# Optimization experiments

Hardware: AMD Instinct MI355X
Metric: run time of the kernel (lower is better)

Reference implementation:

```python
import jax, jax.numpy as jnp
import numpy as np

B, T, BIN, D, S, L = 128, 512, 24, 256, 128, 2
MAX_LEN = 512.0   # config.max_length, used as attention score scale
EPS = 1e-6
P = 3.0           # GeM pooling power


def _sinusoid(t, dim, min_ts=1.0, max_ts=10000.0):
    # half sin / half cos geometric timescales (min_timescale..max_timescale)
    num = dim // 2
    inv = min_ts * jnp.exp(jnp.arange(num, dtype=jnp.float32) * (-np.log(max_ts / min_ts) / max(num - 1, 1)))
    ang = jnp.arange(t, dtype=jnp.float32)[:, None] * inv[None, :]        # [T, dim/2]
    return jnp.concatenate([jnp.sin(ang), jnp.cos(ang)], axis=-1)          # [T, dim]


def _rope(x):
    # rotate-half RoPE over last dim, positions along axis -2
    t, d = x.shape[-2], x.shape[-1]
    inv = 1.0 / (10000.0 ** (jnp.arange(0, d, 2, dtype=jnp.float32) / d))  # [d/2]
    ang = jnp.arange(t, dtype=jnp.float32)[:, None] * inv[None, :]         # [T, d/2]
    sin = jnp.concatenate([jnp.sin(ang), jnp.sin(ang)], axis=-1)
    cos = jnp.concatenate([jnp.cos(ang), jnp.cos(ang)], axis=-1)
    x1, x2 = jnp.split(x, 2, axis=-1)
    return x * cos + jnp.concatenate([-x2, x1], axis=-1) * sin


def setup_inputs() -> dict:
    key = jax.random.key(0)
    ks = jax.random.split(key, 12)
    std_in = 1.0 / np.sqrt(BIN)
    std_d = 1.0 / np.sqrt(D)
    return {
        "x": jax.random.uniform(ks[0], (B, T, BIN), dtype=jnp.float32),
        "pe_scale": jnp.ones((), jnp.float32),                                  # learnable PE scale
        "W_in": jax.random.normal(ks[1], (BIN, D), jnp.float32) * std_in,        # encoder_start
        "b_in": jnp.zeros((D,), jnp.float32),
        "norm_scale": jnp.ones((L,), jnp.float32),                               # ScaledNorm scalar per layer
        "W1": jax.random.normal(ks[2], (L, D, 2 * D + S), jnp.float32) * std_d,  # GAU in-proj
        "b1": jnp.zeros((L, 2 * D + S), jnp.float32),
        "gamma": jnp.ones((L, 2, S), jnp.float32),                               # q/k offset-scale
        "beta": jnp.zeros((L, 2, S), jnp.float32),
        "W2": jax.random.normal(ks[3], (L, D, D), jnp.float32) * std_d,          # GAU out-proj
        "b2": jnp.zeros((L, D), jnp.float32),
        "We": jax.random.normal(ks[4], (D, D), jnp.float32) * std_d,             # metric embedding
        "be": jnp.zeros((D,), jnp.float32),
    }


def reference(x, pe_scale, W_in, b_in, norm_scale, W1, b1, gamma, beta, W2, b2, We, be):
    # scaled sinusoidal positional embedding (additive)
    h = x + pe_scale * _sinusoid(x.shape[1], x.shape[2])
    # encoder start + swish
    h = jax.nn.swish(h @ W_in + b_in)                                   # [B,T,D]
    for i in range(L):  # GAU stack (attention-free gated attention units)
        shortcut = h
        hn = h * jax.lax.rsqrt(jnp.mean(h * h, axis=-1, keepdims=True) + EPS) * norm_scale[i]
        uv = jax.nn.swish(hn @ W1[i] + b1[i])                           # [B,T,2D+S]
        u, v, base = uv[..., :D], uv[..., D:2 * D], uv[..., 2 * D:]
        q = _rope(base * gamma[i, 0] + beta[i, 0])                      # [B,T,S]
        k = _rope(base * gamma[i, 1] + beta[i, 1])
        scores = jnp.einsum('bnd,bmd->bnm', q, k) / MAX_LEN             # [B,T,T]
        attn = jnp.square(jax.nn.relu(scores))                          # SqrReLU
        out = u * jnp.einsum('bnm,bme->bne', attn, v)                   # gated attention output
        h = shortcut + out @ W2[i] + b2[i]
    unpooled = h
    # generalized-mean pooling over sequence (p=3, clamp for stability)
    pooled = jnp.mean(jnp.clip(h, EPS, None) ** P, axis=1) ** (1.0 / P)  # [B,D]
    # metric embedding: linear + L2 normalize
    emb = pooled @ We + be
    emb = emb / jnp.linalg.norm(emb, axis=-1, keepdims=True)
    return emb, unpooled
```

## Files before the change

### kernel.cpp

```cpp
#include <hip/hip_runtime.h>
#include <hip/hip_bf16.h>

#define B_ 128
#define T_ 512
#define BIN_ 24
#define D_ 256
#define S_ 128
#define L_ 2
#define BT_ (B_*T_)

typedef __hip_bfloat16 bf16;
typedef __hip_bfloat162 bf162;
typedef __attribute__((ext_vector_type(8))) short bf16x8;
typedef __attribute__((ext_vector_type(4))) short s16x4;
typedef __attribute__((ext_vector_type(4))) float f32x4;

__device__ __forceinline__ float b2f(bf16 x){ return __bfloat162float(x); }
__device__ __forceinline__ bf16 f2b(float x){ return __float2bfloat16(x); }
__device__ __forceinline__ float swish(float v){
  float e = __builtin_amdgcn_exp2f(-1.442695040888963f * v);
  return v * __builtin_amdgcn_rcpf(1.f + e);
}

__global__ void tables_kernel(const float* pe_scale_ptr, float* pe_tab, float* rs, float* rc) {
  int t = blockIdx.x;
  int j = threadIdx.x;
  float ps = pe_scale_ptr[0];
  const float LOG1E4 = 9.210340371976184f;
  if (j < 64) {
    float inv = expf(-LOG1E4 * (float)j / 64.f);
    float ang = (float)t * inv;
    rs[t*64 + j] = sinf(ang);
    rc[t*64 + j] = cosf(ang);
  }
  if (j < BIN_) {
    int jj = (j < 12) ? j : (j - 12);
    float inv = expf(-LOG1E4 * (float)jj / 11.f);
    float ang = (float)t * inv;
    pe_tab[t*BIN_ + j] = ps * ((j < 12) ? sinf(ang) : cosf(ang));
  }
}

__global__ __launch_bounds__(256) void prep_kernel(const float* W1, const float* W2,
                                                   bf16* W1t, bf16* W2t) {
  int idx = blockIdx.x*256 + threadIdx.x;
  if (idx < 2*256*640) {
    int l = idx / (256*640); int rem = idx % (256*640);
    int k = rem / 640; int n = rem % 640;
    W1t[(size_t)l*640*256 + n*256 + k] = f2b(W1[idx]);
  }
  if (idx < 2*256*256) {
    int l = idx >> 16; int rem = idx & 65535;
    int k = rem >> 8; int n = rem & 255;
    W2t[(size_t)l*65536 + n*256 + k] = f2b(W2[idx]);
  }
}

__global__ __launch_bounds__(256) void init_kernel(float* rms1, float* pooled_raw) {
  int i = blockIdx.x*256 + threadIdx.x;
  if (i < BT_) rms1[i] = 0.f;
  if (i < B_*D_) pooled_raw[i] = 0.f;
}

__global__ __launch_bounds__(256) void embed_kernel(const float* x, const float* pe_tab,
                const float* W_in, const float* b_in, float* h, float* rms0, bf16* hb) {
  __shared__ float xr[8][BIN_];
  __shared__ float wsum[4][8];
  int tid = threadIdx.x;
  int row0 = blockIdx.x * 8;
  if (tid < 8*BIN_) {
    int r = tid / BIN_, k = tid % BIN_;
    int row = row0 + r;
    int t = row & (T_-1);
    xr[r][k] = x[(size_t)row*BIN_ + k] + pe_tab[t*BIN_ + k];
  }
  __syncthreads();
  int d = tid;
  float bi = b_in[d];
  float acc[8];
  #pragma unroll
  for (int r=0;r<8;r++) acc[r]=bi;
  #pragma unroll
  for (int k=0;k<BIN_;k++){
    float w = W_in[k*D_ + d];
    #pragma unroll
    for (int r=0;r<8;r++) acc[r] += xr[r][k]*w;
  }
  float sq[8];
  #pragma unroll
  for (int r=0;r<8;r++){
    float v = swish(acc[r]);
    h[(size_t)(row0+r)*D_ + d] = v;
    hb[(size_t)(row0+r)*D_ + d] = f2b(v);
    sq[r] = v*v;
  }
  #pragma unroll
  for (int off=1; off<64; off<<=1)
    #pragma unroll
    for (int r=0;r<8;r++) sq[r] += __shfl_xor(sq[r], off);
  if ((tid&63)==0)
    #pragma unroll
    for (int r=0;r<8;r++) wsum[tid>>6][r] = sq[r];
  __syncthreads();
  if (tid < 8) rms0[row0+tid] = wsum[0][tid]+wsum[1][tid]+wsum[2][tid]+wsum[3][tid];
}

__global__ __launch_bounds__(256) void gemm1_mfma(const bf16* A, const bf16* Bt,
      const float* bias, const float* rmsraw, const float* norm_scale, int l,
      bf16* u, bf16* Vtg, bf16* basebuf) {
  __shared__ bf16 As[128*72];
  __shared__ bf16 Bs[128*72];
  bf16* Ovl = As;

  int tid = threadIdx.x;
  int w = tid>>6, lane = tid&63, r = lane&15, g = lane>>4;
  int wr = w>>1, wc = w&1;
  int dd = blockIdx.x; int xcd = dd&7, slot = dd>>3;
  int panel = xcd*64 + slot/5; int bx = slot%5;
  int row0 = panel*128, col0 = bx*128;

  f32x4 acc[4][4];
  #pragma unroll
  for (int i=0;i<4;i++)
    #pragma unroll
    for (int j=0;j<4;j++) acc[i][j] = (f32x4){0.f,0.f,0.f,0.f};

  for (int k0=0; k0<D_; k0+=64) {
    #pragma unroll
    for (int i=0;i<4;i++){
      int id = i*256 + tid; int tr = id>>3, tc = id&7;
      *(bf16x8*)(As + tr*72 + tc*8) = *(const bf16x8*)(A  + (size_t)(row0+tr)*D_ + k0 + tc*8);
      *(bf16x8*)(Bs + tr*72 + tc*8) = *(const bf16x8*)(Bt + (size_t)(col0+tr)*D_ + k0 + tc*8);
    }
    __syncthreads();
    #pragma unroll
    for (int kk=0; kk<2; kk++){
      bf16x8 a[4], b[4];
      #pragma unroll
      for (int i=0;i<4;i++){
        a[i] = *(const bf16x8*)(As + (64*wr+16*i+r)*72 + kk*32 + g*8);
        b[i] = *(const bf16x8*)(Bs + (64*wc+16*i+r)*72 + kk*32 + g*8);
      }
      #pragma unroll
      for (int i=0;i<4;i++)
        #pragma unroll
        for (int j=0;j<4;j++)
          acc[i][j] = __builtin_amdgcn_mfma_f32_16x16x32_bf16(a[i], b[j], acc[i][j], 0,0,0);
    }
    __syncthreads();
  }

  float ns = norm_scale[l];
  #pragma unroll
  for (int i=0;i<4;i++){
    size_t grow0 = row0 + 64*wr + 16*i + 4*g;
    float4 rv = *(const float4*)(rmsraw + grow0);
    float sc[4];
    sc[0] = rsqrtf(rv.x*(1.f/D_) + 1e-6f) * ns;
    sc[1] = rsqrtf(rv.y*(1.f/D_) + 1e-6f) * ns;
    sc[2] = rsqrtf(rv.z*(1.f/D_) + 1e-6f) * ns;
    sc[3] = rsqrtf(rv.w*(1.f/D_) + 1e-6f) * ns;
    #pragma unroll
    for (int j=0;j<4;j++){
      int gcol = col0 + 64*wc + 16*j + r;
      float bv = bias[gcol];
      if (bx < 2) {
        #pragma unroll
        for (int reg=0; reg<4; reg++){
          float v = swish(acc[i][j][reg]*sc[reg] + bv);
          u[(grow0+reg)*D_ + gcol] = f2b(v);
        }
      } else if (bx < 4) {
        #pragma unroll
        for (int reg=0; reg<4; reg++){
          float v = swish(acc[i][j][reg]*sc[reg] + bv);
          Ovl[(64*wc+16*j+r)*136 + (64*wr+16*i+4*g+reg)] = f2b(v);
        }
      } else {
        #pragma unroll
        for (int reg=0; reg<4; reg++){
          float v = swish(acc[i][j][reg]*sc[reg] + bv);
          basebuf[(grow0+reg)*S_ + (gcol-512)] = f2b(v);
        }
      }
    }
  }

  if (bx == 2 || bx == 3) {
    __syncthreads();
    size_t bb = row0 >> 9;
    int mg = row0 & 511;
    #pragma unroll
    for (int c=0;c<8;c++){
      int chunk = c*256 + tid;
      int e = chunk >> 4, mloc = (chunk & 15)*8;
      *(bf16x8*)(Vtg + bb*131072 + (size_t)(col0-256+e)*T_ + mg + mloc) =
        *(const bf16x8*)(Ovl + e*136 + mloc);
    }
  }
}

__global__ __launch_bounds__(256) void qk_kernel(const bf16* basebuf, const float* gamma, const float* beta,
      int l, const float* rs, const float* rc, bf16* q, bf16* k) {
  int tid = threadIdx.x;
  int j = tid & 127;
  size_t row = (size_t)blockIdx.x*2 + (tid>>7);
  int t = (int)(row & (T_-1));
  int j2 = j ^ 64;
  float v0 = b2f(basebuf[row*S_ + j]);
  float v1 = b2f(basebuf[row*S_ + j2]);
  int jm = j & 63;
  float sn = rs[t*64 + jm], cs = rc[t*64 + jm];
  float sgn = (j < 64) ? -1.f : 1.f;
  const float* g  = gamma + l*2*S_;
  const float* bt = beta  + l*2*S_;
  float xq = v0*g[j]      + bt[j];
  float pq = v1*g[j2]     + bt[j2];
  q[row*S_ + j] = f2b(xq*cs + sgn*pq*sn);
  float xk = v0*g[S_+j]   + bt[S_+j];
  float pk = v1*g[S_+j2]  + bt[S_+j2];
  k[row*S_ + j] = f2b(xk*cs + sgn*pk*sn);
}

__global__ __launch_bounds__(512, 4) void attn_gemm2_fused(const bf16* q, const bf16* k,
      const bf16* Vtg, const bf16* u, const bf16* W2t, const float* bias,
      float* h, int mode, float* rms1, float* pooled_raw, float* outb, bf16* hb) {
  __shared__ char smem[77824];
  bf16* Ks = (bf16*)smem;
  bf16* Vt = (bf16*)(smem + 17408);
  bf16* Ps = (bf16*)(smem + 50176);
  bf16* Os = (bf16*)smem;
  bf16* Wt = (bf16*)(smem + 67584);

  int tid = threadIdx.x;
  int w = tid >> 6, l = tid & 63;
  int r = l & 15, g = l >> 4;
  int xcd = blockIdx.x & 7, j0 = blockIdx.x >> 3;
  int b  = xcd*16 + (j0 >> 2);
  int nt = j0 & 3;
  size_t rowbase = (size_t)b * T_;
  int n0 = nt * 128;

  bf16x8 qf[4];
  const bf16* qrow = q + (rowbase + n0 + 16*w + r) * S_ + g*8;
  #pragma unroll
  for (int kk=0; kk<4; kk++) qf[kk] = *(const bf16x8*)(qrow + kk*32);

  f32x4 oacc[16];
  #pragma unroll
  for (int i=0;i<16;i++) oacc[i] = (f32x4){0.f,0.f,0.f,0.f};

  for (int m0 = 0; m0 < T_; m0 += 64) {
    #pragma unroll
    for (int i=0;i<2;i++){
      int chunk = i*512 + tid;
      int row = chunk >> 4, c = chunk & 15;
      *(bf16x8*)(Ks + row*136 + c*8) =
        *(const bf16x8*)(k + (rowbase + m0 + row)*S_ + c*8);
    }
    #pragma unroll
    for (int i=0;i<4;i++){
      int chunk = i*512 + tid;
      int e = chunk >> 3, c = chunk & 7;
      *(bf16x8*)(Vt + e*64 + ((c ^ (e&7)) << 3)) =
        *(const bf16x8*)(Vtg + (size_t)b*131072 + (size_t)e*T_ + m0 + c*8);
    }
    __syncthreads();

    #pragma unroll
    for (int nf=0; nf<4; nf++){
      f32x4 sacc = (f32x4){0.f,0.f,0.f,0.f};
      #pragma unroll
      for (int kk=0; kk<4; kk++){
        bf16x8 kf = *(const bf16x8*)(Ks + (16*nf + r)*136 + kk*32 + g*8);
        sacc = __builtin_amdgcn_mfma_f32_16x16x32_bf16(qf[kk], kf, sacc, 0,0,0);
      }
      #pragma unroll
      for (int reg=0; reg<4; reg++){
        float t = fmaxf(sacc[reg] * (1.f/512.f), 0.f);
        Ps[(16*w + 4*g + reg)*72 + 16*nf + r] = f2b(t*t);
      }
    }
    #pragma unroll
    for (int ks=0; ks<2; ks++){
      bf16x8 pa = *(const bf16x8*)(Ps + (16*w + r)*72 + ks*32 + g*8);
      #pragma unroll
      for (int nf2=0; nf2<16; nf2++){
        int e = 16*nf2 + r;
        bf16x8 vb = *(const bf16x8*)(Vt + e*64 + (((4*ks + g) ^ (e&7)) << 3));
        oacc[nf2] = __builtin_amdgcn_mfma_f32_16x16x32_bf16(pa, vb, oacc[nf2], 0,0,0);
      }
    }
    __syncthreads();
  }

  size_t growbase = rowbase + n0;
  #pragma unroll
  for (int nf2=0; nf2<16; nf2++){
    #pragma unroll
    for (int reg=0; reg<4; reg++){
      int row = 16*w + 4*g + reg;
      int col = 16*nf2 + r;
      float uv = b2f(u[(growbase + row)*D_ + col]);
      Os[row*264 + col] = f2b(oacc[nf2][reg] * uv);
    }
  }
  #pragma unroll
  for (int i=0;i<16;i++) oacc[i] = (f32x4){0.f,0.f,0.f,0.f};
  for (int kc=0; kc<8; kc++){
    bf16x8 a0 = *(const bf16x8*)(Os + (16*w + r)*264 + kc*32 + g*8);
    #pragma unroll
    for (int nh=0; nh<2; nh++){
      __syncthreads();
      {
        int rowW = tid>>2, ko = (tid&3)*8;
        *(bf16x8*)(Wt + rowW*40 + ko) =
          *(const bf16x8*)(W2t + (size_t)(128*nh + rowW)*256 + kc*32 + ko);
      }
      __syncthreads();
      #pragma unroll
      for (int nf2h=0; nf2h<8; nf2h++){
        bf16x8 bfr = *(const bf16x8*)(Wt + (16*nf2h + r)*40 + g*8);
        oacc[nh*8+nf2h] =
          __builtin_amdgcn_mfma_f32_16x16x32_bf16(a0, bfr, oacc[nh*8+nf2h], 0,0,0);
      }
    }
  }

  if (mode == 0) {
    #pragma unroll
    for (int reg=0; reg<4; reg++){
      size_t row = growbase + 16*w + 4*g + reg;
      float ssum = 0.f;
      #pragma unroll
      for (int nf2=0; nf2<16; nf2++){
        int col = 16*nf2 + r;
        float hv = h[row*D_ + col] + oacc[nf2][reg] + bias[col];
        h[row*D_ + col] = hv;
        hb[row*D_ + col] = f2b(hv);
        ssum += hv*hv;
      }
      ssum += __shfl_xor(ssum,1); ssum += __shfl_xor(ssum,2);
      ssum += __shfl_xor(ssum,4); ssum += __shfl_xor(ssum,8);
      if (r == 0) rms1[row] = ssum;
    }
  } else {
    #pragma unroll
    for (int nf2=0; nf2<16; nf2++){
      int col = 16*nf2 + r;
      float bv = bias[col];
      float psum = 0.f;
      #pragma unroll
      for (int reg=0; reg<4; reg++){
        size_t row = growbase + 16*w + 4*g + reg;
        float hv = h[row*D_ + col] + oacc[nf2][reg] + bv;
        outb[row*D_ + col] = hv;
        float cv = fmaxf(hv, 1e-6f);
        psum += cv*cv*cv;
      }
      psum += __shfl_xor(psum,16); psum += __shfl_xor(psum,32);
      if (g == 0) atomicAdd(pooled_raw + b*D_ + col, psum);
    }
  }
}

__global__ __launch_bounds__(256) void emb_kernel(const float* pooled_raw, const float* We,
      const float* be, float* out) {
  __shared__ float pr[D_];
  __shared__ float red[256];
  int b = blockIdx.x, j = threadIdx.x;
  pr[j] = cbrtf(pooled_raw[b*D_+j] * (1.f/T_));
  __syncthreads();
  float acc = be[j];
  for (int kk=0;kk<D_;kk++) acc += pr[kk]*We[kk*D_+j];
  red[j] = acc*acc;
  __syncthreads();
  for (int off=128; off>0; off>>=1){
    if (j<off) red[j]+=red[j+off];
    __syncthreads();
  }
  out[b*D_+j] = acc * rsqrtf(red[0]);
}

extern "C" void kernel_launch(void* const* d_in, const int* in_sizes, int n_in,
                              void* d_out, int out_size, void* d_ws, size_t ws_size,
                              hipStream_t stream) {
  const float* x         = (const float*)d_in[0];
  const float* pe_scale  = (const float*)d_in[1];
  const float* W_in      = (const float*)d_in[2];
  const float* b_in      = (const float*)d_in[3];
  const float* norm_scale= (const float*)d_in[4];
  const float* W1        = (const float*)d_in[5];
  const float* b1        = (const float*)d_in[6];
  const float* gamma     = (const float*)d_in[7];
  const float* beta      = (const float*)d_in[8];
  const float* W2        = (const float*)d_in[9];
  const float* b2        = (const float*)d_in[10];
  const float* We        = (const float*)d_in[11];
  const float* be        = (const float*)d_in[12];

  char* ws = (char*)d_ws;
  float* h       = (float*)(ws);
  bf16*  hb      = (bf16*)(ws + 67108864);
  bf16*  u       = (bf16*)(ws + 100663296);
  bf16*  Vtg     = (bf16*)(ws + 134217728);
  bf16*  basebuf = (bf16*)(ws + 167772160);
  bf16*  q       = (bf16*)(ws + 184549376);
  bf16*  kbuf    = (bf16*)(ws + 201326592);
  float* pe_tab  = (float*)(ws + 218103808);
  float* rs_tab  = (float*)(ws + 218152960);
  float* rc_tab  = (float*)(ws + 218284032);
  float* pooled_raw = (float*)(ws + 218415104);
  float* rms0    = (float*)(ws + 218546176);
  float* rms1    = (float*)(ws + 218808320);
  bf16*  W1t     = (bf16*)(ws + 219070464);
  bf16*  W2t     = (bf16*)(ws + 219725824);

  tables_kernel<<<T_, 64, 0, stream>>>(pe_scale, pe_tab, rs_tab, rc_tab);
  prep_kernel<<<1280, 256, 0, stream>>>(W1, W2, W1t, W2t);
  init_kernel<<<BT_/256, 256, 0, stream>>>(rms1, pooled_raw);
  embed_kernel<<<BT_/8, 256, 0, stream>>>(x, pe_tab, W_in, b_in, h, rms0, hb);
  float* outb = (float*)d_out + B_*D_;
  for (int l=0; l<L_; l++) {
    gemm1_mfma<<<BT_/128*5, 256, 0, stream>>>(hb, W1t + (size_t)l*640*D_, b1 + l*640,
        l ? rms1 : rms0, norm_scale, l, u, Vtg, basebuf);
    qk_kernel<<<BT_/2, 256, 0, stream>>>(basebuf, gamma, beta, l, rs_tab, rc_tab, q, kbuf);
    attn_gemm2_fused<<<B_*4, 512, 0, stream>>>(q, kbuf, Vtg, u,
        W2t + (size_t)l*D_*D_, b2 + l*D_, h, l, rms1, pooled_raw, outb, hb);
  }
  emb_kernel<<<B_, 256, 0, stream>>>(pooled_raw, We, be, (float*)d_out);
}
```

Before: 378.3 us.

## Fuse q/k offset-scale and RoPE into gemm1 epilogue; vectorize u gating

Result: slower. 415.0 us (+9.7%).

```diff
diff --git a/kernel.cpp b/kernel.cpp
--- a/kernel.cpp
+++ b/kernel.cpp
@@ -107,7 +107,8 @@
 
 __global__ __launch_bounds__(256) void gemm1_mfma(const bf16* A, const bf16* Bt,
       const float* bias, const float* rmsraw, const float* norm_scale, int l,
-      bf16* u, bf16* Vtg, bf16* basebuf) {
+      const float* gamma, const float* beta, const float* rs, const float* rc,
+      bf16* u, bf16* Vtg, bf16* q, bf16* k) {
   __shared__ bf16 As[128*72];
   __shared__ bf16 Bs[128*72];
   bf16* Ovl = As;
@@ -180,7 +181,7 @@
         #pragma unroll
         for (int reg=0; reg<4; reg++){
           float v = swish(acc[i][j][reg]*sc[reg] + bv);
-          basebuf[(grow0+reg)*S_ + (gcol-512)] = f2b(v);
+          Ovl[(64*wr+16*i+4*g+reg)*136 + (64*wc+16*j+r)] = f2b(v);
         }
       }
     }
@@ -197,29 +198,40 @@
       *(bf16x8*)(Vtg + bb*131072 + (size_t)(col0-256+e)*T_ + mg + mloc) =
         *(const bf16x8*)(Ovl + e*136 + mloc);
     }
-  }
-}
-
-__global__ __launch_bounds__(256) void qk_kernel(const bf16* basebuf, const float* gamma, const float* beta,
-      int l, const float* rs, const float* rc, bf16* q, bf16* k) {
-  int tid = threadIdx.x;
-  int j = tid & 127;
-  size_t row = (size_t)blockIdx.x*2 + (tid>>7);
-  int t = (int)(row & (T_-1));
-  int j2 = j ^ 64;
-  float v0 = b2f(basebuf[row*S_ + j]);
-  float v1 = b2f(basebuf[row*S_ + j2]);
-  int jm = j & 63;
-  float sn = rs[t*64 + jm], cs = rc[t*64 + jm];
-  float sgn = (j < 64) ? -1.f : 1.f;
-  const float* g  = gamma + l*2*S_;
-  const float* bt = beta  + l*2*S_;
-  float xq = v0*g[j]      + bt[j];
-  float pq = v1*g[j2]     + bt[j2];
-  q[row*S_ + j] = f2b(xq*cs + sgn*pq*sn);
-  float xk = v0*g[S_+j]   + bt[S_+j];
-  float pk = v1*g[S_+j2]  + bt[S_+j2];
-  k[row*S_ + j] = f2b(xk*cs + sgn*pk*sn);
+  } else if (bx == 4) {
+    __syncthreads();
+    int lrow = tid>>1, h64 = (tid&1)*64;
+    size_t grow = row0 + lrow;
+    int t = (int)(grow & (T_-1));
+    const float* rsb = rs + t*64;
+    const float* rcb = rc + t*64;
+    const float* gg = gamma + l*2*S_;
+    const float* bt = beta  + l*2*S_;
+    #pragma unroll
+    for (int c=0;c<8;c++){
+      int j0 = h64 + c*8;
+      bf16x8 xj = *(const bf16x8*)(Ovl + lrow*136 + j0);
+      bf16x8 xo = *(const bf16x8*)(Ovl + lrow*136 + (j0^64));
+      bf16x8 qo, ko;
+      #pragma unroll
+      for (int e=0;e<8;e++){
+        int j = j0 + e;
+        int jm = j & 63;
+        float sn = rsb[jm], cs = rcb[jm];
+        float sgn = (j < 64) ? -1.f : 1.f;
+        float v0 = b2f(((bf16*)&xj)[e]);
+        float v1 = b2f(((bf16*)&xo)[e]);
+        float xq = v0*gg[j]      + bt[j];
+        float pq = v1*gg[j^64]   + bt[j^64];
+        ((bf16*)&qo)[e] = f2b(xq*cs + sgn*pq*sn);
+        float xk = v0*gg[S_+j]       + bt[S_+j];
+        float pk = v1*gg[S_+(j^64)]  + bt[S_+(j^64)];
+        ((bf16*)&ko)[e] = f2b(xk*cs + sgn*pk*sn);
+      }
+      *(bf16x8*)(q + grow*S_ + j0) = qo;
+      *(bf16x8*)(k + grow*S_ + j0) = ko;
+    }
+  }
 }
 
 __global__ __launch_bounds__(512, 4) void attn_gemm2_fused(const bf16* q, const bf16* k,
@@ -299,14 +311,26 @@
   for (int nf2=0; nf2<16; nf2++){
     #pragma unroll
     for (int reg=0; reg<4; reg++){
-      int row = 16*w + 4*g + reg;
-      int col = 16*nf2 + r;
-      float uv = b2f(u[(growbase + row)*D_ + col]);
-      Os[row*264 + col] = f2b(oacc[nf2][reg] * uv);
-    }
+      Os[(16*w + 4*g + reg)*264 + 16*nf2 + r] = f2b(oacc[nf2][reg]);
+    }
+  }
+  __syncthreads();
+  #pragma unroll
+  for (int i=0;i<8;i++){
+    int chunk = i*512 + tid;
+    int row = chunk >> 5, c = chunk & 31;
+    bf16x8 uvv = *(const bf16x8*)(u + (growbase + row)*D_ + c*8);
+    bf16x8 ov  = *(const bf16x8*)(Os + row*264 + c*8);
+    bf16x8 res;
+    #pragma unroll
+    for (int e=0;e<8;e++)
+      ((bf16*)&res)[e] = f2b(b2f(((bf16*)&ov)[e]) * b2f(((bf16*)&uvv)[e]));
+    *(bf16x8*)(Os + row*264 + c*8) = res;
   }
   #pragma unroll
   for (int i=0;i<16;i++) oacc[i] = (f32x4){0.f,0.f,0.f,0.f};
+  __syncthreads();
+
   for (int kc=0; kc<8; kc++){
     bf16x8 a0 = *(const bf16x8*)(Os + (16*w + r)*264 + kc*32 + g*8);
     #pragma unroll
@@ -404,7 +428,6 @@
   bf16*  hb      = (bf16*)(ws + 67108864);
   bf16*  u       = (bf16*)(ws + 100663296);
   bf16*  Vtg     = (bf16*)(ws + 134217728);
-  bf16*  basebuf = (bf16*)(ws + 167772160);
   bf16*  q       = (bf16*)(ws + 184549376);
   bf16*  kbuf    = (bf16*)(ws + 201326592);
   float* pe_tab  = (float*)(ws + 218103808);
@@ -423,8 +446,7 @@
   float* outb = (float*)d_out + B_*D_;
   for (int l=0; l<L_; l++) {
     gemm1_mfma<<<BT_/128*5, 256, 0, stream>>>(hb, W1t + (size_t)l*640*D_, b1 + l*640,
-        l ? rms1 : rms0, norm_scale, l, u, Vtg, basebuf);
-    qk_kernel<<<BT_/2, 256, 0, stream>>>(basebuf, gamma, beta, l, rs_tab, rc_tab, q, kbuf);
+        l ? rms1 : rms0, norm_scale, l, gamma, beta, rs_tab, rc_tab, u, Vtg, q, kbuf);
     attn_gemm2_fused<<<B_*4, 512, 0, stream>>>(q, kbuf, Vtg, u,
         W2t + (size_t)l*D_*D_, b2 + l*D_, h, l, rms1, pooled_raw, outb, hb);
   }
```
